# Kernel optimization log

Hardware: AMD Instinct MI355X
Metric: run time of the kernel (lower is better)

Reference implementation:

```python
import jax, jax.numpy as jnp
import numpy as np

IH, IW = 48, 48           # img_size
C = 256                   # inp == oup
NH, HD = 8, 32            # num_heads, head_dims; inner_dim = 256
HID = 4 * C               # MLP hidden
N = IH * IW               # window size (seq len) = 2304
SCALE = (C // NH) ** -0.5 # (inp_dims // num_heads) ** -0.5
EPS = 1e-5


def _relative_position_index():
    coords = np.stack(np.meshgrid(np.arange(IH), np.arange(IW), indexing='ij'))
    cf = coords.reshape(2, -1)
    rel = (cf[:, :, None] - cf[:, None, :]).transpose(1, 2, 0)
    rel[:, :, 0] += IH - 1
    rel[:, :, 1] += IW - 1
    rel[:, :, 0] *= 2 * IW - 1
    return jnp.asarray(rel.sum(-1).astype(np.int32))  # [N, N]


def setup_inputs() -> dict:
    key = jax.random.key(0)
    ks = jax.random.split(key, 12)
    s = 0.02
    return {
        'x': jax.random.normal(ks[0], (1, IH, IW, C), jnp.float32),
        'gamma1': jnp.ones((C,), jnp.float32),
        'beta1': jnp.zeros((C,), jnp.float32),
        'w_qkv': jax.random.normal(ks[1], (C, 3 * NH * HD), jnp.float32) * s,
        'w_proj': jax.random.normal(ks[2], (NH * HD, C), jnp.float32) * s,
        'b_proj': jnp.zeros((C,), jnp.float32),
        'bias_table': jax.random.normal(ks[3], ((2 * IH - 1) * (2 * IW - 1), NH), jnp.float32) * s,
        'gamma2': jnp.ones((C,), jnp.float32),
        'beta2': jnp.zeros((C,), jnp.float32),
        'w_fc1': jax.random.normal(ks[4], (C, HID), jnp.float32) * s,
        'b_fc1': jnp.zeros((HID,), jnp.float32),
        'w_fc2': jax.random.normal(ks[5], (HID, C), jnp.float32) * s,
        'b_fc2': jnp.zeros((C,), jnp.float32),
        'rel_idx': _relative_position_index(),
    }


def _layernorm(x, g, b):
    mu = jnp.mean(x, axis=-1, keepdims=True)
    var = jnp.mean(jnp.square(x - mu), axis=-1, keepdims=True)
    return (x - mu) * jax.lax.rsqrt(var + EPS) * g + b


def reference(x, gamma1, beta1, w_qkv, w_proj, b_proj, bias_table,
              gamma2, beta2, w_fc1, b_fc1, w_fc2, b_fc2, rel_idx):
    shortcut = x                                   # [1, IH, IW, C]
    t = x.reshape(1, N, C)
    t = _layernorm(t, gamma1, beta1)

    # qkv: [1, N, 3*NH*HD] -> q, k, v each [1, NH, N, HD]
    qkv = (t @ w_qkv).reshape(1, N, 3, NH, HD).transpose(2, 0, 3, 1, 4)
    q, k, v = qkv[0], qkv[1], qkv[2]
    q = q * SCALE

    attn = jnp.einsum('bhnd,bhmd->bhnm', q, k)     # [1, NH, N, N]
    # relative position bias: gather table rows by index -> [NH, N, N]
    bias = bias_table[rel_idx.reshape(-1)].reshape(N, N, NH).transpose(2, 0, 1)
    attn = jax.nn.softmax(attn + bias[None], axis=-1)

    o = jnp.einsum('bhnm,bhmd->bhnd', attn, v)     # [1, NH, N, HD]
    o = o.transpose(0, 2, 1, 3).reshape(1, N, NH * HD)
    o = o @ w_proj + b_proj                        # [1, N, C]

    x = shortcut + o.reshape(1, IH, IW, C)
    shortcut = x

    t = _layernorm(x.reshape(1, N, C), gamma2, beta2)
    t = jax.nn.gelu(t @ w_fc1 + b_fc1, approximate=False) @ w_fc2 + b_fc2
    return shortcut + t.reshape(1, IH, IW, C)
```

## Files before the change

### kernel.cpp

```cpp
#include <hip/hip_runtime.h>
#include <hip/hip_bf16.h>

typedef __bf16 bf16x8 __attribute__((__ext_vector_type__(8)));
typedef __bf16 bf16x4 __attribute__((__ext_vector_type__(4)));
typedef float  f32x4  __attribute__((__ext_vector_type__(4)));

#define MFMA16(a, b, c) __builtin_amdgcn_mfma_f32_16x16x32_bf16((a), (b), (c), 0, 0, 0)

static constexpr int   NSEQ  = 2304;
static constexpr float SCALE = 0.17677669529663687f;
static constexpr int   KVS   = 6;

#define SWZ(row, colByte) ((row) * 512 + ((colByte) ^ (((row) & 7) << 4)))

__global__ __launch_bounds__(256) void prep_kernel(
    const float* __restrict__ wqkv, const float* __restrict__ wproj,
    const float* __restrict__ wfc1, const float* __restrict__ wfc2,
    const float* __restrict__ btab,
    __hip_bfloat16* __restrict__ oqkv, __hip_bfloat16* __restrict__ oproj,
    __hip_bfloat16* __restrict__ ofc1, __hip_bfloat16* __restrict__ ofc2,
    float* __restrict__ btabT)
{
    int b = blockIdx.x;
    int tid = threadIdx.x;
    if (b >= 768) {
        int base = (b - 768) * 1024;
        for (int k = tid; k < 1024; k += 256) {
            int e = base + k;
            if (e < 72200) { int i = e >> 3, hh = e & 7; btabT[hh * 9025 + i] = btab[e]; }
        }
        return;
    }
    const float* src; __hip_bfloat16* dst; int K, N, t;
    if (b < 192)      { src = wqkv;  dst = oqkv;  K = 256;  N = 768;  t = b;       }
    else if (b < 256) { src = wproj; dst = oproj; K = 256;  N = 256;  t = b - 192; }
    else if (b < 512) { src = wfc1;  dst = ofc1;  K = 256;  N = 1024; t = b - 256; }
    else              { src = wfc2;  dst = ofc2;  K = 1024; N = 256;  t = b - 512; }
    int ntn = N >> 5;
    int tk = t / ntn, tn = t % ntn;
    __shared__ float tile[32][33];
    int tx = tid & 31, ty = tid >> 5;
    #pragma unroll
    for (int r = 0; r < 4; ++r)
        tile[ty + 8 * r][tx] = src[(size_t)(tk * 32 + ty + 8 * r) * N + tn * 32 + tx];
    __syncthreads();
    #pragma unroll
    for (int r = 0; r < 4; ++r)
        dst[(size_t)(tn * 32 + ty + 8 * r) * K + tk * 32 + tx] =
            __float2bfloat16(tile[tx][ty + 8 * r]);
}

__global__ __launch_bounds__(256) void qkv_ln_kernel(
    const float* __restrict__ x, const float* __restrict__ g1,
    const float* __restrict__ b1, const __hip_bfloat16* __restrict__ BT,
    __hip_bfloat16* __restrict__ Qb, __hip_bfloat16* __restrict__ Kb,
    __hip_bfloat16* __restrict__ Vt)
{
    __shared__ char smem[64 * 512];
    int tid = threadIdx.x;
    int w = tid >> 6, lane = tid & 63, l15 = lane & 15, g = lane >> 4;
    int bm = blockIdx.y * 64, bn = blockIdx.x * 64;

    {
        int row = tid >> 2;
        int part = tid & 3;
        const float* xr = x + (size_t)(bm + row) * 256 + part * 64;
        float vals[64];
        float s = 0.f, s2 = 0.f;
        #pragma unroll
        for (int i = 0; i < 16; ++i) {
            f32x4 v4 = *reinterpret_cast<const f32x4*>(xr + 4 * i);
            #pragma unroll
            for (int e = 0; e < 4; ++e) {
                vals[4 * i + e] = v4[e];
                s += v4[e]; s2 += v4[e] * v4[e];
            }
        }
        s  += __shfl_xor(s, 1);  s  += __shfl_xor(s, 2);
        s2 += __shfl_xor(s2, 1); s2 += __shfl_xor(s2, 2);
        float mu   = s * (1.f / 256.f);
        float var  = s2 * (1.f / 256.f) - mu * mu;
        float rstd = rsqrtf(var + 1e-5f);
        #pragma unroll
        for (int i = 0; i < 16; ++i) {
            int c = part * 64 + 4 * i;
            f32x4 gv = *reinterpret_cast<const f32x4*>(g1 + c);
            f32x4 bv = *reinterpret_cast<const f32x4*>(b1 + c);
            bf16x4 pk;
            #pragma unroll
            for (int e = 0; e < 4; ++e)
                pk[e] = (__bf16)((vals[4 * i + e] - mu) * rstd * gv[e] + bv[e]);
            *reinterpret_cast<bf16x4*>(smem + SWZ(row, c * 2)) = pk;
        }
    }
    __syncthreads();

    int wr = w >> 1, wc = w & 1;
    f32x4 acc[2][2];
    #pragma unroll
    for (int i = 0; i < 2; ++i)
        #pragma unroll
        for (int j = 0; j < 2; ++j) acc[i][j] = (f32x4){0.f, 0.f, 0.f, 0.f};
    const __hip_bfloat16* Brow = BT + (size_t)(bn + wc * 32 + l15) * 256 + 8 * g;
    #pragma unroll
    for (int kb = 0; kb < 256; kb += 32) {
        bf16x8 af[2], bfr[2];
        #pragma unroll
        for (int i = 0; i < 2; ++i)
            af[i] = *reinterpret_cast<const bf16x8*>(
                smem + SWZ(wr * 32 + 16 * i + l15, (kb + 8 * g) * 2));
        #pragma unroll
        for (int j = 0; j < 2; ++j)
            bfr[j] = *reinterpret_cast<const bf16x8*>(Brow + (size_t)16 * j * 256 + kb);
        #pragma unroll
        for (int i = 0; i < 2; ++i)
            #pragma unroll
            for (int j = 0; j < 2; ++j)
                acc[i][j] = MFMA16(af[i], bfr[j], acc[i][j]);
    }

    if (bn >= 512) {
        __syncthreads();
        float* vtile = (float*)smem;
        #pragma unroll
        for (int fi = 0; fi < 2; ++fi)
        #pragma unroll
        for (int fj = 0; fj < 2; ++fj)
        #pragma unroll
        for (int j = 0; j < 4; ++j)
            vtile[(32 * wr + 16 * fi + 4 * g + j) * 65 + 32 * wc + 16 * fj + l15] =
                acc[fi][fj][j];
        __syncthreads();
        for (int e = tid; e < 4096; e += 256) {
            int mi = e & 63, ni = e >> 6;
            int n = bn + ni;
            int h = (n >> 5) & 7, d = n & 31;
            Vt[(size_t)(h * 32 + d) * NSEQ + bm + mi] = __float2bfloat16(vtile[mi * 65 + ni]);
        }
        return;
    }
    #pragma unroll
    for (int fi = 0; fi < 2; ++fi)
    #pragma unroll
    for (int fj = 0; fj < 2; ++fj)
    #pragma unroll
    for (int j = 0; j < 4; ++j) {
        int m = bm + 32 * wr + 16 * fi + 4 * g + j;
        int n = bn + 32 * wc + 16 * fj + l15;
        float v = acc[fi][fj][j];
        int which = n >> 8, h = (n >> 5) & 7, d = n & 31;
        if (which == 0) Qb[((size_t)(h * NSEQ + m) << 5) + d] = __float2bfloat16(v * SCALE);
        else            Kb[((size_t)(h * NSEQ + m) << 5) + d] = __float2bfloat16(v);
    }
}

__global__ __launch_bounds__(256) void attn_kernel(
    const __hip_bfloat16* __restrict__ Q,
    const __hip_bfloat16* __restrict__ Kb,
    const __hip_bfloat16* __restrict__ Vt,
    const float* __restrict__ btabT,
    float* __restrict__ Pm, float* __restrict__ Pl,
    __hip_bfloat16* __restrict__ PO)
{
    __shared__ float bias_l[10 * 96];
    __shared__ __hip_bfloat16 P_lds[4][16][72];

    int bid = blockIdx.x;
    int h = bid / (36 * KVS);
    int r = bid - h * (36 * KVS);
    int qt = r / KVS, kvq = r - qt * KVS;
    int tid = threadIdx.x;
    int w = tid >> 6, lane = tid & 63, l15 = lane & 15, g = lane >> 4;

    int q0 = qt * 64;
    int i1min = q0 / 48, i1max = (q0 + 63) / 48;
    int i2min = kvq * 8;
    int dimin = i1min - (i2min + 7);
    int nrow = (i1max - i1min) + 8;

    for (int i = tid; i < nrow * 95; i += 256) {
        int rr = i / 95, cc = i - rr * 95;
        bias_l[rr * 96 + cc] = btabT[h * 9025 + (dimin + rr + 47) * 95 + cc];
    }
    __syncthreads();

    int qrow = q0 + w * 16 + l15;
    int i1 = qrow / 48, j1 = qrow - i1 * 48;
    int laneBase = (i1 - dimin) * 96 + j1 + 47;
    bf16x8 qf = *reinterpret_cast<const bf16x8*>(Q + ((size_t)(h * NSEQ + qrow) << 5) + 8 * g);

    float m_st = -1e30f, l_st = 0.f;
    f32x4 o0 = (f32x4){0.f, 0.f, 0.f, 0.f};
    f32x4 o1 = (f32x4){0.f, 0.f, 0.f, 0.f};
    const f32x4 zero = (f32x4){0.f, 0.f, 0.f, 0.f};
    int kvbase = kvq * 384;

    for (int t = 0; t < 6; ++t) {
        int kv0 = kvbase + t * 64;
        bf16x8 vf[4];
        #pragma unroll
        for (int u = 0; u < 4; ++u) {
            int dt = u >> 1, hh = u & 1;
            vf[u] = *reinterpret_cast<const bf16x8*>(
                Vt + (size_t)((h << 5) + 16 * dt + l15) * NSEQ + kv0 + 32 * hh + 8 * g);
        }
        f32x4 st[4];
        #pragma unroll
        for (int s = 0; s < 4; ++s) {
            bf16x8 kf = *reinterpret_cast<const bf16x8*>(
                Kb + ((size_t)(h * NSEQ + kv0 + 16 * s + l15) << 5) + 8 * g);
            st[s] = MFMA16(kf, qf, zero);
        }
        float mx = -1e30f;
        #pragma unroll
        for (int s = 0; s < 4; ++s) {
            int kvb = kv0 + 16 * s + 4 * g;
            int i2 = kvb / 48;
            int j2b = kvb - 48 * i2;
            int sub = laneBase - i2 * 96 - j2b;
            #pragma unroll
            for (int j = 0; j < 4; ++j) {
                int idx = sub - j - ((j2b + j >= 48) ? 48 : 0);
                float sv = st[s][j] + bias_l[idx];
                st[s][j] = sv;
                mx = fmaxf(mx, sv);
            }
        }
        mx = fmaxf(mx, __shfl_xor(mx, 16));
        mx = fmaxf(mx, __shfl_xor(mx, 32));
        float mn = fmaxf(m_st, mx);
        float rs = 0.f;
        #pragma unroll
        for (int s = 0; s < 4; ++s)
            #pragma unroll
            for (int j = 0; j < 4; ++j) {
                float e = __expf(st[s][j] - mn);
                st[s][j] = e;
                rs += e;
            }
        rs += __shfl_xor(rs, 16);
        rs += __shfl_xor(rs, 32);
        float sc = __expf(m_st - mn);
        l_st = l_st * sc + rs;
        m_st = mn;
        float scr[4];
        #pragma unroll
        for (int j = 0; j < 4; ++j) scr[j] = __shfl(sc, 4 * g + j);
        #pragma unroll
        for (int j = 0; j < 4; ++j) { o0[j] *= scr[j]; o1[j] *= scr[j]; }
        #pragma unroll
        for (int s = 0; s < 4; ++s) {
            bf16x4 pk = { (__bf16)st[s][0], (__bf16)st[s][1], (__bf16)st[s][2], (__bf16)st[s][3] };
            *reinterpret_cast<bf16x4*>(&P_lds[w][l15][16 * s + 4 * g]) = pk;
        }
        #pragma unroll
        for (int hh = 0; hh < 2; ++hh) {
            bf16x8 pf = *reinterpret_cast<const bf16x8*>(&P_lds[w][l15][32 * hh + 8 * g]);
            o0 = MFMA16(pf, vf[hh], o0);
            o1 = MFMA16(pf, vf[2 + hh], o1);
        }
    }

    size_t mb = (size_t)(kvq * 8 + h) * NSEQ;
    if (g == 0) { Pm[mb + qrow] = m_st; Pl[mb + qrow] = l_st; }
    #pragma unroll
    for (int dt = 0; dt < 2; ++dt)
        #pragma unroll
        for (int j = 0; j < 4; ++j) {
            int row = q0 + w * 16 + 4 * g + j;
            PO[(mb + row) * 32 + 16 * dt + l15] =
                __float2bfloat16(dt == 0 ? o0[j] : o1[j]);
        }
}

__global__ __launch_bounds__(512) void proj_kernel(
    const __hip_bfloat16* __restrict__ PO, const float* __restrict__ Pm,
    const float* __restrict__ Pl, const __hip_bfloat16* __restrict__ BT,
    const float* __restrict__ bproj, const float* __restrict__ x,
    const float* __restrict__ g2, const float* __restrict__ b2,
    float* __restrict__ x2, __hip_bfloat16* __restrict__ t2)
{
    __shared__ char smem[16 * 512];
    __shared__ float redS[8][16], redQ[8][16], muA[16], rsA[16];
    int tid = threadIdx.x;
    int q0 = blockIdx.x * 16;

    {
        int row = tid >> 5;
        int c0  = (tid & 31) * 8;
        int h = c0 >> 5, d = c0 & 31;
        float m[KVS], l[KVS], a[KVS];
        #pragma unroll
        for (int k = 0; k < KVS; ++k) {
            size_t mb = (size_t)(k * 8 + h) * NSEQ + q0 + row;
            m[k] = Pm[mb]; l[k] = Pl[mb];
        }
        float M = m[0];
        #pragma unroll
        for (int k = 1; k < KVS; ++k) M = fmaxf(M, m[k]);
        float L = 0.f;
        #pragma unroll
        for (int k = 0; k < KVS; ++k) { a[k] = __expf(m[k] - M); L += a[k] * l[k]; }
        float inv = 1.f / L;
        float o[8] = {0.f, 0.f, 0.f, 0.f, 0.f, 0.f, 0.f, 0.f};
        #pragma unroll
        for (int k = 0; k < KVS; ++k) {
            bf16x8 po = *reinterpret_cast<const bf16x8*>(
                PO + ((size_t)(k * 8 + h) * NSEQ + q0 + row) * 32 + d);
            #pragma unroll
            for (int e = 0; e < 8; ++e) o[e] += a[k] * (float)po[e];
        }
        bf16x8 pk;
        #pragma unroll
        for (int e = 0; e < 8; ++e) pk[e] = (__bf16)(o[e] * inv);
        *reinterpret_cast<bf16x8*>(smem + SWZ(row, c0 * 2)) = pk;
    }
    __syncthreads();

    int w = tid >> 6, lane = tid & 63, l15 = lane & 15, g = lane >> 4;
    f32x4 acc[2];
    acc[0] = (f32x4){0.f, 0.f, 0.f, 0.f};
    acc[1] = (f32x4){0.f, 0.f, 0.f, 0.f};
    const __hip_bfloat16* Brow = BT + (size_t)(w * 32 + l15) * 256 + 8 * g;
    #pragma unroll
    for (int kb = 0; kb < 256; kb += 32) {
        bf16x8 af = *reinterpret_cast<const bf16x8*>(smem + SWZ(l15, (kb + 8 * g) * 2));
        #pragma unroll
        for (int fj = 0; fj < 2; ++fj) {
            bf16x8 bfr = *reinterpret_cast<const bf16x8*>(Brow + (size_t)16 * fj * 256 + kb);
            acc[fj] = MFMA16(af, bfr, acc[fj]);
        }
    }

    float rr[2][4];
    float s[4] = {0.f, 0.f, 0.f, 0.f}, sq[4] = {0.f, 0.f, 0.f, 0.f};
    #pragma unroll
    for (int fj = 0; fj < 2; ++fj)
        #pragma unroll
        for (int j = 0; j < 4; ++j) {
            int mrow = 4 * g + j;
            int n = w * 32 + 16 * fj + l15;
            float v = acc[fj][j] + bproj[n] + x[(size_t)(q0 + mrow) * 256 + n];
            x2[(size_t)(q0 + mrow) * 256 + n] = v;
            rr[fj][j] = v;
            s[j] += v; sq[j] += v * v;
        }
    #pragma unroll
    for (int mask = 1; mask <= 8; mask <<= 1)
        #pragma unroll
        for (int j = 0; j < 4; ++j) {
            s[j]  += __shfl_xor(s[j],  mask);
            sq[j] += __shfl_xor(sq[j], mask);
        }
    if (l15 == 0)
        #pragma unroll
        for (int j = 0; j < 4; ++j) { redS[w][4 * g + j] = s[j]; redQ[w][4 * g + j] = sq[j]; }
    __syncthreads();
    if (tid < 16) {
        float S = 0.f, Qq = 0.f;
        #pragma unroll
        for (int ww = 0; ww < 8; ++ww) { S += redS[ww][tid]; Qq += redQ[ww][tid]; }
        float mu = S * (1.f / 256.f);
        float var = Qq * (1.f / 256.f) - mu * mu;
        muA[tid] = mu;
        rsA[tid] = rsqrtf(var + 1e-5f);
    }
    __syncthreads();
    #pragma unroll
    for (int fj = 0; fj < 2; ++fj)
        #pragma unroll
        for (int j = 0; j < 4; ++j) {
            int mrow = 4 * g + j;
            int n = w * 32 + 16 * fj + l15;
            float tv = (rr[fj][j] - muA[mrow]) * rsA[mrow] * g2[n] + b2[n];
            t2[(size_t)(q0 + mrow) * 256 + n] = __float2bfloat16(tv);
        }
}

template <int EPI, int NN, int KK, int FM, int FN, int WR, int WC>
__global__ __launch_bounds__(256) void gemm_kernel(
    const __hip_bfloat16* __restrict__ A,
    const __hip_bfloat16* __restrict__ BT,
    const float* __restrict__ bias,
    const float* __restrict__ resid,
    void* __restrict__ out0)
{
    constexpr int BM = WR * FM * 16, BN = WC * FN * 16;
    int bm = blockIdx.y * BM, bn = blockIdx.x * BN;
    int tid = threadIdx.x;
    int w = tid >> 6, lane = tid & 63, l15 = lane & 15, g = lane >> 4;
    int wr = w / WC, wc = w % WC;

    f32x4 acc[FM][FN];
    #pragma unroll
    for (int i = 0; i < FM; ++i)
        #pragma unroll
        for (int j = 0; j < FN; ++j) acc[i][j] = (f32x4){0.f, 0.f, 0.f, 0.f};

    const __hip_bfloat16* Arow = A  + (size_t)(bm + wr * FM * 16 + l15) * KK + 8 * g;
    const __hip_bfloat16* Brow = BT + (size_t)(bn + wc * FN * 16 + l15) * KK + 8 * g;

    #pragma unroll
    for (int kb = 0; kb < KK; kb += 32) {
        bf16x8 af[FM], bfr[FN];
        #pragma unroll
        for (int i = 0; i < FM; ++i)
            af[i] = *reinterpret_cast<const bf16x8*>(Arow + (size_t)16 * i * KK + kb);
        #pragma unroll
        for (int j = 0; j < FN; ++j)
            bfr[j] = *reinterpret_cast<const bf16x8*>(Brow + (size_t)16 * j * KK + kb);
        #pragma unroll
        for (int i = 0; i < FM; ++i)
            #pragma unroll
            for (int j = 0; j < FN; ++j)
                acc[i][j] = MFMA16(af[i], bfr[j], acc[i][j]);
    }

    #pragma unroll
    for (int fi = 0; fi < FM; ++fi)
    #pragma unroll
    for (int fj = 0; fj < FN; ++fj)
    #pragma unroll
    for (int j = 0; j < 4; ++j) {
        int m = bm + wr * FM * 16 + 16 * fi + 4 * g + j;
        int n = bn + wc * FN * 16 + 16 * fj + l15;
        float v = acc[fi][fj][j];
        if constexpr (EPI == 2) {
            float r = v + bias[n];
            r = 0.5f * r * (1.f + erff(r * 0.70710678118654752f));
            ((__hip_bfloat16*)out0)[(size_t)m * NN + n] = __float2bfloat16(r);
        } else {
            ((float*)out0)[(size_t)m * 256 + n] = v + bias[n] + resid[(size_t)m * 256 + n];
        }
    }
}

extern "C" void kernel_launch(void* const* d_in, const int* in_sizes, int n_in,
                              void* d_out, int out_size, void* d_ws, size_t ws_size,
                              hipStream_t stream)
{
    const float* x      = (const float*)d_in[0];
    const float* gamma1 = (const float*)d_in[1];
    const float* beta1  = (const float*)d_in[2];
    const float* w_qkv  = (const float*)d_in[3];
    const float* w_proj = (const float*)d_in[4];
    const float* b_proj = (const float*)d_in[5];
    const float* btab   = (const float*)d_in[6];
    const float* gamma2 = (const float*)d_in[7];
    const float* beta2  = (const float*)d_in[8];
    const float* w_fc1  = (const float*)d_in[9];
    const float* b_fc1  = (const float*)d_in[10];
    const float* w_fc2  = (const float*)d_in[11];
    const float* b_fc2  = (const float*)d_in[12];

    char* ws = (char*)d_ws;
    size_t off = 0;
    auto alloc = [&](size_t bytes) -> void* {
        void* p = ws + off;
        off += (bytes + 255) & ~(size_t)255;
        return p;
    };
    __hip_bfloat16* wqkvT = (__hip_bfloat16*)alloc((size_t)768 * 256 * 2);
    __hip_bfloat16* wprojT= (__hip_bfloat16*)alloc((size_t)256 * 256 * 2);
    __hip_bfloat16* wfc1T = (__hip_bfloat16*)alloc((size_t)1024 * 256 * 2);
    __hip_bfloat16* wfc2T = (__hip_bfloat16*)alloc((size_t)256 * 1024 * 2);
    float*          btabT = (float*)alloc((size_t)8 * 9025 * 4);
    __hip_bfloat16* Qb    = (__hip_bfloat16*)alloc((size_t)8 * NSEQ * 32 * 2);
    __hip_bfloat16* Kbuf  = (__hip_bfloat16*)alloc((size_t)8 * NSEQ * 32 * 2);
    __hip_bfloat16* Vt    = (__hip_bfloat16*)alloc((size_t)8 * 32 * NSEQ * 2);
    float*          x2    = (float*)alloc((size_t)NSEQ * 256 * 4);
    __hip_bfloat16* t2    = (__hip_bfloat16*)alloc((size_t)NSEQ * 256 * 2);
    float*          Pm    = (float*)alloc((size_t)KVS * 8 * NSEQ * 4);
    float*          Pl    = (float*)alloc((size_t)KVS * 8 * NSEQ * 4);
    __hip_bfloat16* PO    = (__hip_bfloat16*)alloc((size_t)KVS * 8 * NSEQ * 32 * 2);
    __hip_bfloat16* hb    = (__hip_bfloat16*)alloc((size_t)NSEQ * 1024 * 2);

    prep_kernel<<<dim3(839), dim3(256), 0, stream>>>(
        w_qkv, w_proj, w_fc1, w_fc2, btab, wqkvT, wprojT, wfc1T, wfc2T, btabT);

    qkv_ln_kernel<<<dim3(12, 36), dim3(256), 0, stream>>>(
        x, gamma1, beta1, wqkvT, Qb, Kbuf, Vt);

    attn_kernel<<<dim3(8 * 36 * KVS), dim3(256), 0, stream>>>(
        Qb, Kbuf, Vt, btabT, Pm, Pl, PO);

    proj_kernel<<<dim3(144), dim3(512), 0, stream>>>(
        PO, Pm, Pl, wprojT, b_proj, x, gamma2, beta2, x2, t2);

    gemm_kernel<2, 1024, 256, 2, 2, 2, 2><<<dim3(16, 36), dim3(256), 0, stream>>>(
        t2, wfc1T, b_fc1, nullptr, hb);

    gemm_kernel<3, 256, 1024, 1, 1, 4, 1><<<dim3(16, 36), dim3(256), 0, stream>>>(
        hb, wfc2T, b_fc2, x2, d_out);
}
```

Measured before the change: 192.2 us.

## Software-pipeline GEMM loads, split-K fc2 with atomics, shrink qkv tiles, add setprio

Several changes land together. The qkv, proj and generic GEMM loops now double-buffer their global B/A fragment loads so loads overlap with MFMA. The fc2 GEMM is split four ways along K and accumulates into the output with atomicAdd, and the fc1 kernel pre-initialises the output with residual plus bias. The qkv_ln tile shrinks to 32 rows to launch more blocks, and s_setprio brackets the MFMA sections in attention. The extra parallelism and latency hiding cost atomic traffic, redundant LN work, and a non-deterministic summation order.

```diff
diff --git a/kernel.cpp b/kernel.cpp
--- a/kernel.cpp
+++ b/kernel.cpp
@@ -56,19 +56,17 @@
     __hip_bfloat16* __restrict__ Qb, __hip_bfloat16* __restrict__ Kb,
     __hip_bfloat16* __restrict__ Vt)
 {
-    __shared__ char smem[64 * 512];
+    __shared__ char smem[32 * 512];
     int tid = threadIdx.x;
-    int w = tid >> 6, lane = tid & 63, l15 = lane & 15, g = lane >> 4;
-    int bm = blockIdx.y * 64, bn = blockIdx.x * 64;
+    int bn = blockIdx.x * 64, bm = blockIdx.y * 32;
 
     {
-        int row = tid >> 2;
-        int part = tid & 3;
-        const float* xr = x + (size_t)(bm + row) * 256 + part * 64;
-        float vals[64];
+        int row = tid >> 3, part = tid & 7;
+        const float* xr = x + (size_t)(bm + row) * 256 + part * 32;
+        float vals[32];
         float s = 0.f, s2 = 0.f;
         #pragma unroll
-        for (int i = 0; i < 16; ++i) {
+        for (int i = 0; i < 8; ++i) {
             f32x4 v4 = *reinterpret_cast<const f32x4*>(xr + 4 * i);
             #pragma unroll
             for (int e = 0; e < 4; ++e) {
@@ -76,14 +74,14 @@
                 s += v4[e]; s2 += v4[e] * v4[e];
             }
         }
-        s  += __shfl_xor(s, 1);  s  += __shfl_xor(s, 2);
-        s2 += __shfl_xor(s2, 1); s2 += __shfl_xor(s2, 2);
+        s  += __shfl_xor(s, 1);  s  += __shfl_xor(s, 2);  s  += __shfl_xor(s, 4);
+        s2 += __shfl_xor(s2, 1); s2 += __shfl_xor(s2, 2); s2 += __shfl_xor(s2, 4);
         float mu   = s * (1.f / 256.f);
         float var  = s2 * (1.f / 256.f) - mu * mu;
         float rstd = rsqrtf(var + 1e-5f);
         #pragma unroll
-        for (int i = 0; i < 16; ++i) {
-            int c = part * 64 + 4 * i;
+        for (int i = 0; i < 8; ++i) {
+            int c = part * 32 + 4 * i;
             f32x4 gv = *reinterpret_cast<const f32x4*>(g1 + c);
             f32x4 bv = *reinterpret_cast<const f32x4*>(b1 + c);
             bf16x4 pk;
@@ -95,44 +93,46 @@
     }
     __syncthreads();
 
+    int w = tid >> 6, lane = tid & 63, l15 = lane & 15, g = lane >> 4;
     int wr = w >> 1, wc = w & 1;
-    f32x4 acc[2][2];
-    #pragma unroll
-    for (int i = 0; i < 2; ++i)
-        #pragma unroll
-        for (int j = 0; j < 2; ++j) acc[i][j] = (f32x4){0.f, 0.f, 0.f, 0.f};
+    f32x4 acc[2];
+    acc[0] = (f32x4){0.f, 0.f, 0.f, 0.f};
+    acc[1] = (f32x4){0.f, 0.f, 0.f, 0.f};
     const __hip_bfloat16* Brow = BT + (size_t)(bn + wc * 32 + l15) * 256 + 8 * g;
-    #pragma unroll
-    for (int kb = 0; kb < 256; kb += 32) {
-        bf16x8 af[2], bfr[2];
-        #pragma unroll
-        for (int i = 0; i < 2; ++i)
-            af[i] = *reinterpret_cast<const bf16x8*>(
-                smem + SWZ(wr * 32 + 16 * i + l15, (kb + 8 * g) * 2));
-        #pragma unroll
-        for (int j = 0; j < 2; ++j)
-            bfr[j] = *reinterpret_cast<const bf16x8*>(Brow + (size_t)16 * j * 256 + kb);
-        #pragma unroll
-        for (int i = 0; i < 2; ++i)
-            #pragma unroll
-            for (int j = 0; j < 2; ++j)
-                acc[i][j] = MFMA16(af[i], bfr[j], acc[i][j]);
-    }
+    bf16x8 p0[2][2], p1[2][2];
+
+#define QLOADB(dst, kb) { \
+    _Pragma("unroll") for (int ks = 0; ks < 2; ++ks) \
+    _Pragma("unroll") for (int fj = 0; fj < 2; ++fj) \
+        dst[ks][fj] = *reinterpret_cast<const bf16x8*>(Brow + (size_t)16 * fj * 256 + (kb) + 32 * ks); }
+#define QCOMP(src, kb) { \
+    _Pragma("unroll") for (int ks = 0; ks < 2; ++ks) { \
+        bf16x8 af = *reinterpret_cast<const bf16x8*>(smem + SWZ(wr * 16 + l15, 2 * ((kb) + 32 * ks + 8 * g))); \
+        _Pragma("unroll") for (int fj = 0; fj < 2; ++fj) \
+            acc[fj] = MFMA16(af, src[ks][fj], acc[fj]); } }
+
+    QLOADB(p0, 0);
+    QLOADB(p1, 64);
+    QCOMP(p0, 0);
+    QLOADB(p0, 128);
+    QCOMP(p1, 64);
+    QLOADB(p1, 192);
+    QCOMP(p0, 128);
+    QCOMP(p1, 192);
+#undef QLOADB
+#undef QCOMP
 
     if (bn >= 512) {
         __syncthreads();
         float* vtile = (float*)smem;
         #pragma unroll
-        for (int fi = 0; fi < 2; ++fi)
-        #pragma unroll
         for (int fj = 0; fj < 2; ++fj)
         #pragma unroll
         for (int j = 0; j < 4; ++j)
-            vtile[(32 * wr + 16 * fi + 4 * g + j) * 65 + 32 * wc + 16 * fj + l15] =
-                acc[fi][fj][j];
+            vtile[(wr * 16 + 4 * g + j) * 65 + wc * 32 + 16 * fj + l15] = acc[fj][j];
         __syncthreads();
-        for (int e = tid; e < 4096; e += 256) {
-            int mi = e & 63, ni = e >> 6;
+        for (int e = tid; e < 2048; e += 256) {
+            int mi = e & 31, ni = e >> 5;
             int n = bn + ni;
             int h = (n >> 5) & 7, d = n & 31;
             Vt[(size_t)(h * 32 + d) * NSEQ + bm + mi] = __float2bfloat16(vtile[mi * 65 + ni]);
@@ -140,14 +140,12 @@
         return;
     }
     #pragma unroll
-    for (int fi = 0; fi < 2; ++fi)
-    #pragma unroll
     for (int fj = 0; fj < 2; ++fj)
     #pragma unroll
     for (int j = 0; j < 4; ++j) {
-        int m = bm + 32 * wr + 16 * fi + 4 * g + j;
-        int n = bn + 32 * wc + 16 * fj + l15;
-        float v = acc[fi][fj][j];
+        int m = bm + wr * 16 + 4 * g + j;
+        int n = bn + wc * 32 + 16 * fj + l15;
+        float v = acc[fj][j];
         int which = n >> 8, h = (n >> 5) & 7, d = n & 31;
         if (which == 0) Qb[((size_t)(h * NSEQ + m) << 5) + d] = __float2bfloat16(v * SCALE);
         else            Kb[((size_t)(h * NSEQ + m) << 5) + d] = __float2bfloat16(v);
@@ -205,12 +203,14 @@
                 Vt + (size_t)((h << 5) + 16 * dt + l15) * NSEQ + kv0 + 32 * hh + 8 * g);
         }
         f32x4 st[4];
+        __builtin_amdgcn_s_setprio(1);
         #pragma unroll
         for (int s = 0; s < 4; ++s) {
             bf16x8 kf = *reinterpret_cast<const bf16x8*>(
                 Kb + ((size_t)(h * NSEQ + kv0 + 16 * s + l15) << 5) + 8 * g);
             st[s] = MFMA16(kf, qf, zero);
         }
+        __builtin_amdgcn_s_setprio(0);
         float mx = -1e30f;
         #pragma unroll
         for (int s = 0; s < 4; ++s) {
@@ -253,12 +253,14 @@
             bf16x4 pk = { (__bf16)st[s][0], (__bf16)st[s][1], (__bf16)st[s][2], (__bf16)st[s][3] };
             *reinterpret_cast<bf16x4*>(&P_lds[w][l15][16 * s + 4 * g]) = pk;
         }
+        __builtin_amdgcn_s_setprio(1);
         #pragma unroll
         for (int hh = 0; hh < 2; ++hh) {
             bf16x8 pf = *reinterpret_cast<const bf16x8*>(&P_lds[w][l15][32 * hh + 8 * g]);
             o0 = MFMA16(pf, vf[hh], o0);
             o1 = MFMA16(pf, vf[2 + hh], o1);
         }
+        __builtin_amdgcn_s_setprio(0);
     }
 
     size_t mb = (size_t)(kvq * 8 + h) * NSEQ;
@@ -322,15 +324,28 @@
     acc[0] = (f32x4){0.f, 0.f, 0.f, 0.f};
     acc[1] = (f32x4){0.f, 0.f, 0.f, 0.f};
     const __hip_bfloat16* Brow = BT + (size_t)(w * 32 + l15) * 256 + 8 * g;
-    #pragma unroll
-    for (int kb = 0; kb < 256; kb += 32) {
-        bf16x8 af = *reinterpret_cast<const bf16x8*>(smem + SWZ(l15, (kb + 8 * g) * 2));
-        #pragma unroll
-        for (int fj = 0; fj < 2; ++fj) {
-            bf16x8 bfr = *reinterpret_cast<const bf16x8*>(Brow + (size_t)16 * fj * 256 + kb);
-            acc[fj] = MFMA16(af, bfr, acc[fj]);
-        }
-    }
+    bf16x8 p0[2][2], p1[2][2];
+
+#define PLOADB(dst, kb) { \
+    _Pragma("unroll") for (int ks = 0; ks < 2; ++ks) \
+    _Pragma("unroll") for (int fj = 0; fj < 2; ++fj) \
+        dst[ks][fj] = *reinterpret_cast<const bf16x8*>(Brow + (size_t)16 * fj * 256 + (kb) + 32 * ks); }
+#define PCOMP(src, kb) { \
+    _Pragma("unroll") for (int ks = 0; ks < 2; ++ks) { \
+        bf16x8 af = *reinterpret_cast<const bf16x8*>(smem + SWZ(l15, 2 * ((kb) + 32 * ks + 8 * g))); \
+        _Pragma("unroll") for (int fj = 0; fj < 2; ++fj) \
+            acc[fj] = MFMA16(af, src[ks][fj], acc[fj]); } }
+
+    PLOADB(p0, 0);
+    PLOADB(p1, 64);
+    PCOMP(p0, 0);
+    PLOADB(p0, 128);
+    PCOMP(p1, 64);
+    PLOADB(p1, 192);
+    PCOMP(p0, 128);
+    PCOMP(p1, 192);
+#undef PLOADB
+#undef PCOMP
 
     float rr[2][4];
     float s[4] = {0.f, 0.f, 0.f, 0.f}, sq[4] = {0.f, 0.f, 0.f, 0.f};
@@ -377,44 +392,67 @@
         }
 }
 
-template <int EPI, int NN, int KK, int FM, int FN, int WR, int WC>
+template <int EPI, int NN, int KTOT, int FM, int FN, int WR, int WC>
 __global__ __launch_bounds__(256) void gemm_kernel(
     const __hip_bfloat16* __restrict__ A,
     const __hip_bfloat16* __restrict__ BT,
     const float* __restrict__ bias,
     const float* __restrict__ resid,
-    void* __restrict__ out0)
+    const float* __restrict__ bias2,
+    void* __restrict__ out0,
+    float* __restrict__ outPre)
 {
     constexpr int BM = WR * FM * 16, BN = WC * FN * 16;
     int bm = blockIdx.y * BM, bn = blockIdx.x * BN;
+    int k0 = blockIdx.z * 256;
     int tid = threadIdx.x;
     int w = tid >> 6, lane = tid & 63, l15 = lane & 15, g = lane >> 4;
     int wr = w / WC, wc = w % WC;
 
+    if constexpr (EPI == 2) {
+        if (blockIdx.x == 0) {
+            for (int e = tid; e < BM * 64; e += 256) {
+                int mi = e >> 6, c4 = (e & 63) << 2;
+                f32x4 xv = *reinterpret_cast<const f32x4*>(resid + (size_t)(bm + mi) * 256 + c4);
+                f32x4 bv = *reinterpret_cast<const f32x4*>(bias2 + c4);
+                *reinterpret_cast<f32x4*>(outPre + (size_t)(bm + mi) * 256 + c4) = xv + bv;
+            }
+        }
+    }
+
     f32x4 acc[FM][FN];
     #pragma unroll
     for (int i = 0; i < FM; ++i)
         #pragma unroll
         for (int j = 0; j < FN; ++j) acc[i][j] = (f32x4){0.f, 0.f, 0.f, 0.f};
 
-    const __hip_bfloat16* Arow = A  + (size_t)(bm + wr * FM * 16 + l15) * KK + 8 * g;
-    const __hip_bfloat16* Brow = BT + (size_t)(bn + wc * FN * 16 + l15) * KK + 8 * g;
-
-    #pragma unroll
-    for (int kb = 0; kb < KK; kb += 32) {
-        bf16x8 af[FM], bfr[FN];
-        #pragma unroll
-        for (int i = 0; i < FM; ++i)
-            af[i] = *reinterpret_cast<const bf16x8*>(Arow + (size_t)16 * i * KK + kb);
-        #pragma unroll
-        for (int j = 0; j < FN; ++j)
-            bfr[j] = *reinterpret_cast<const bf16x8*>(Brow + (size_t)16 * j * KK + kb);
-        #pragma unroll
-        for (int i = 0; i < FM; ++i)
-            #pragma unroll
-            for (int j = 0; j < FN; ++j)
-                acc[i][j] = MFMA16(af[i], bfr[j], acc[i][j]);
-    }
+    const __hip_bfloat16* Arow = A  + (size_t)(bm + wr * FM * 16 + l15) * KTOT + k0 + 8 * g;
+    const __hip_bfloat16* Brow = BT + (size_t)(bn + wc * FN * 16 + l15) * KTOT + k0 + 8 * g;
+
+    bf16x8 a0[2][FM], b0[2][FN], a1[2][FM], b1[2][FN];
+
+#define GLOAD(ar, br, kb) { \
+    _Pragma("unroll") for (int ks = 0; ks < 2; ++ks) { \
+        _Pragma("unroll") for (int i = 0; i < FM; ++i) \
+            ar[ks][i] = *reinterpret_cast<const bf16x8*>(Arow + (size_t)16 * i * KTOT + (kb) + 32 * ks); \
+        _Pragma("unroll") for (int j2 = 0; j2 < FN; ++j2) \
+            br[ks][j2] = *reinterpret_cast<const bf16x8*>(Brow + (size_t)16 * j2 * KTOT + (kb) + 32 * ks); } }
+#define GCOMP(ar, br) { \
+    _Pragma("unroll") for (int ks = 0; ks < 2; ++ks) \
+        _Pragma("unroll") for (int i = 0; i < FM; ++i) \
+            _Pragma("unroll") for (int j2 = 0; j2 < FN; ++j2) \
+                acc[i][j2] = MFMA16(ar[ks][i], br[ks][j2], acc[i][j2]); }
+
+    GLOAD(a0, b0, 0);
+    GLOAD(a1, b1, 64);
+    GCOMP(a0, b0);
+    GLOAD(a0, b0, 128);
+    GCOMP(a1, b1);
+    GLOAD(a1, b1, 192);
+    GCOMP(a0, b0);
+    GCOMP(a1, b1);
+#undef GLOAD
+#undef GCOMP
 
     #pragma unroll
     for (int fi = 0; fi < FM; ++fi)
@@ -430,7 +468,7 @@
             r = 0.5f * r * (1.f + erff(r * 0.70710678118654752f));
             ((__hip_bfloat16*)out0)[(size_t)m * NN + n] = __float2bfloat16(r);
         } else {
-            ((float*)out0)[(size_t)m * 256 + n] = v + bias[n] + resid[(size_t)m * 256 + n];
+            atomicAdd((float*)out0 + (size_t)m * 256 + n, v);
         }
     }
 }
@@ -478,7 +516,7 @@
     prep_kernel<<<dim3(839), dim3(256), 0, stream>>>(
         w_qkv, w_proj, w_fc1, w_fc2, btab, wqkvT, wprojT, wfc1T, wfc2T, btabT);
 
-    qkv_ln_kernel<<<dim3(12, 36), dim3(256), 0, stream>>>(
+    qkv_ln_kernel<<<dim3(12, 72), dim3(256), 0, stream>>>(
         x, gamma1, beta1, wqkvT, Qb, Kbuf, Vt);
 
     attn_kernel<<<dim3(8 * 36 * KVS), dim3(256), 0, stream>>>(
@@ -487,9 +525,9 @@
     proj_kernel<<<dim3(144), dim3(512), 0, stream>>>(
         PO, Pm, Pl, wprojT, b_proj, x, gamma2, beta2, x2, t2);
 
-    gemm_kernel<2, 1024, 256, 2, 2, 2, 2><<<dim3(16, 36), dim3(256), 0, stream>>>(
-        t2, wfc1T, b_fc1, nullptr, hb);
-
-    gemm_kernel<3, 256, 1024, 1, 1, 4, 1><<<dim3(16, 36), dim3(256), 0, stream>>>(
-        hb, wfc2T, b_fc2, x2, d_out);
+    gemm_kernel<2, 1024, 256, 2, 1, 2, 2><<<dim3(32, 36), dim3(256), 0, stream>>>(
+        t2, wfc1T, b_fc1, x2, b_fc2, hb, (float*)d_out);
+
+    gemm_kernel<3, 256, 1024, 1, 1, 4, 1><<<dim3(16, 36, 4), dim3(256), 0, stream>>>(
+        hb, wfc2T, b_fc2, nullptr, nullptr, d_out, nullptr);
 }
```

Measured after the change: 211.7 us. +10.2%, slower.
